# Performance work log

Hardware: AMD Instinct MI355X
Metric: run time of the kernel (lower is better)

## Reference

```python
import jax, jax.numpy as jnp
import numpy as np

BN_EPS = 1e-5


def _poly_ste(x):
    # Piecewise polynomial surrogate used for the activation STE backward:
    #   x < -1        -> -1
    #   x >= 1        -> 1
    out = jnp.where(x < -1, -1.0, x * x + 2.0 * x)
    out = jnp.where(x < 0, out, -x * x + 2.0 * x)
    out = jnp.where(x < 1, out, 1.0)
    return out


def setup_inputs() -> dict:
    key = jax.random.key(0)
    ks = jax.random.split(key, 7)
    N, C, H, W = 32, 128, 56, 56
    P = 128  # planes
    return {
        "x": jax.random.normal(ks[0], (N, C, H, W), dtype=jnp.float32),
        "weight": jax.random.normal(ks[1], (P, C, 3, 3), dtype=jnp.float32) * 0.05,
        "bias": jax.random.normal(ks[2], (P,), dtype=jnp.float32) * 0.05,
        "gamma": jax.random.uniform(ks[3], (P,), dtype=jnp.float32, minval=0.5, maxval=1.5),
        "beta": jax.random.normal(ks[4], (P,), dtype=jnp.float32) * 0.05,
        "running_mean": jax.random.normal(ks[5], (P,), dtype=jnp.float32) * 0.1,
        "running_var": jax.random.uniform(ks[6], (P,), dtype=jnp.float32, minval=0.5, maxval=1.5),
    }


def reference(x, weight, bias, gamma, beta, running_mean, running_var):
    # BinaryActivation: forward = sign(x), backward = d(poly)/dx (STE via detach trick)
    poly = _poly_ste(x)
    a = poly + jax.lax.stop_gradient(jnp.sign(x) - poly)

    # HardBinaryConv: weights binarized with straight-through sign; input already +/-1.
    wb = weight + jax.lax.stop_gradient(jnp.sign(weight) - weight)

    # 3x3 conv, stride 1, padding 1, NCHW / OIHW layout
    out = jax.lax.conv_general_dilated(
        a, wb,
        window_strides=(1, 1),
        padding=((1, 1), (1, 1)),
        dimension_numbers=("NCHW", "OIHW", "NCHW"),
    )
    out = out + bias[None, :, None, None]

    # BatchNorm2d in eval mode (running statistics)
    inv = gamma / jnp.sqrt(running_var + BN_EPS)
    out = out * inv[None, :, None, None] + (beta - running_mean * inv)[None, :, None, None]

    # Residual add (downsample=None, stride=1, inplanes==planes)
    return out + x
```

## Files before the change

kernel.cpp:

```cpp
#include <hip/hip_runtime.h>
#include <stdint.h>

#define N_  32
#define C_  128
#define H_  56
#define W_  56
#define HW_ 3136
#define P_  128

using i32x4 = __attribute__((ext_vector_type(4))) int;

#define WI8_BYTES (P_*1152)

__global__ __launch_bounds__(256) void wpack_kernel(const float* __restrict__ weight,
        const float* __restrict__ bias, const float* __restrict__ gamma,
        const float* __restrict__ beta, const float* __restrict__ mean,
        const float* __restrict__ var,
        uint32_t* __restrict__ wI8, float* __restrict__ invG, float* __restrict__ b0G) {
    int gid = blockIdx.x * 256 + threadIdx.x;
    int p   = gid / 288;
    int rem = gid % 288;
    int k   = rem * 4;
    int tp  = k >> 7;
    int c   = k & 127;
    uint32_t d = 0;
    #pragma unroll
    for (int i2 = 0; i2 < 4; ++i2) {
        float v = weight[((size_t)p * C_ + c + i2) * 9 + tp];
        uint32_t by = (v >= 0.f) ? 0x01u : 0xFFu;
        d |= by << (8 * i2);
    }
    wI8[gid] = d;
    if (blockIdx.x == 0 && threadIdx.x < P_) {
        int pp = threadIdx.x;
        float inv = gamma[pp] * rsqrtf(var[pp] + 1e-5f);
        invG[pp] = inv;
        b0G[pp]  = bias[pp] * inv + beta[pp] - mean[pp] * inv;
    }
}

__global__ __launch_bounds__(256) void bconv_kernel(
        const uint4* __restrict__ wI8v,
        const float* __restrict__ invG, const float* __restrict__ b0G,
        const float* __restrict__ x, float* __restrict__ out) {
    __shared__ uint4 actT[4 * 68 * 8];
    __shared__ float sInv[P_], sB0[P_];

    int tid = threadIdx.x;
    int bid = (blockIdx.x & 7) * 112 + (blockIdx.x >> 3);
    int img = bid / 28;
    int rp  = bid % 28;
    int r0  = rp * 2;

    int lane = tid & 63;
    int wi   = tid >> 6;
    int q    = lane >> 4;
    int l15  = lane & 15;
    int m0   = wi * 32;

    if (tid < P_) { sInv[tid] = invG[tid]; sB0[tid] = b0G[tid]; }

    const uint4* wbase = wI8v + (size_t)(m0 + l15) * 72;
    i32x4 aw[2][2][2];
    #pragma unroll
    for (int mi = 0; mi < 2; ++mi)
        #pragma unroll
        for (int ks = 0; ks < 2; ++ks)
            aw[0][mi][ks] = *(const i32x4*)&wI8v[(size_t)(m0 + mi*16 + l15) * 72
                                                 + ks * 4 + q];

    if (tid < 224) {
        int rho = tid / 56;
        int rr2 = tid % 56;
        int cg  = rr2 / 14;
        int tq  = rr2 % 14;
        int h   = r0 - 1 + rho;
        bool vh = ((unsigned)h < (unsigned)H_);
        uint32_t c0 = vh ? 0x01010101u : 0u;
        uint32_t cf = vh ? 0xFEu       : 0u;
        const uint32_t* xb = (const uint32_t*)x
            + ((size_t)img * C_ + cg * 32) * HW_ + (vh ? h : 0) * W_ + tq * 4;
        int colL0 = tq * 4 + 1;
        #pragma unroll
        for (int ph = 0; ph < 2; ++ph) {
            uint32_t cell0[4], cell1[4], cell2[4], cell3[4];
            #pragma unroll
            for (int d = 0; d < 4; ++d) {
                uint32_t w0 = 0, w1 = 0, w2 = 0, w3 = 0;
                if (vh) {
                    #pragma unroll
                    for (int i = 0; i < 4; ++i) {
                        uint4 u = *(const uint4*)(xb + (size_t)(ph * 16 + d * 4 + i) * HW_);
                        uint32_t sh = i * 8;
                        w0 |= (u.x >> 31) << sh;
                        w1 |= (u.y >> 31) << sh;
                        w2 |= (u.z >> 31) << sh;
                        w3 |= (u.w >> 31) << sh;
                    }
                }
                cell0[d] = c0 + w0 * cf;
                cell1[d] = c0 + w1 * cf;
                cell2[d] = c0 + w2 * cf;
                cell3[d] = c0 + w3 * cf;
            }
            int cb = cg * 2 + ph;
            actT[(rho * 68 + colL0 + 0) * 8 + (cb ^ ((colL0 + 0) & 7))] =
                make_uint4(cell0[0], cell0[1], cell0[2], cell0[3]);
            actT[(rho * 68 + colL0 + 1) * 8 + (cb ^ ((colL0 + 1) & 7))] =
                make_uint4(cell1[0], cell1[1], cell1[2], cell1[3]);
            actT[(rho * 68 + colL0 + 2) * 8 + (cb ^ ((colL0 + 2) & 7))] =
                make_uint4(cell2[0], cell2[1], cell2[2], cell2[3]);
            actT[(rho * 68 + colL0 + 3) * 8 + (cb ^ ((colL0 + 3) & 7))] =
                make_uint4(cell3[0], cell3[1], cell3[2], cell3[3]);
        }
    } else {
        int z = tid - 224;
        #pragma unroll
        for (int rep = 0; rep < 2; ++rep) {
            int e = z + rep * 32;
            if (e < 48) {
                int rho  = e / 12;
                int jj   = e % 12;
                int colL = jj ? (56 + jj) : 0;
                int base = (rho * 68 + colL) * 8;
                #pragma unroll
                for (int s = 0; s < 8; ++s) actT[base + s] = make_uint4(0u,0u,0u,0u);
            }
        }
    }

    __syncthreads();

    i32x4 acc[2][8];
    #pragma unroll
    for (int mi = 0; mi < 2; ++mi)
        #pragma unroll
        for (int j = 0; j < 8; ++j)
            #pragma unroll
            for (int e = 0; e < 4; ++e) acc[mi][j][e] = 0;

    #pragma unroll 1
    for (int t9 = 0; t9 < 9; ++t9) {
        int nb = t9 & 1;
        if (t9 < 8) {
            #pragma unroll
            for (int mi = 0; mi < 2; ++mi)
                #pragma unroll
                for (int ks = 0; ks < 2; ++ks)
                    aw[nb ^ 1][mi][ks] = *(const i32x4*)&wI8v[(size_t)(m0 + mi*16 + l15) * 72
                                                              + (t9 + 1) * 8 + ks * 4 + q];
        }
        int dh = t9 / 3, dw = t9 % 3;
        #pragma unroll
        for (int ks = 0; ks < 2; ++ks) {
            #pragma unroll
            for (int j = 0; j < 8; ++j) {
                int n    = j * 16 + l15;
                int colL = (n & 63) + dw;
                int rho  = (n >> 6) + dh;
                i32x4 bf = *(const i32x4*)&actT[(rho * 68 + colL) * 8 + ((ks * 4 + q) ^ (colL & 7))];
                acc[0][j] = __builtin_amdgcn_mfma_i32_16x16x64_i8(aw[nb][0][ks], bf, acc[0][j], 0, 0, 0);
                acc[1][j] = __builtin_amdgcn_mfma_i32_16x16x64_i8(aw[nb][1][ks], bf, acc[1][j], 0, 0, 0);
            }
        }
    }

    __syncthreads();

    float* S = (float*)actT + wi * (16 * 132);
    #pragma unroll
    for (int mi = 0; mi < 2; ++mi) {
        float invR[4], b0R[4];
        #pragma unroll
        for (int reg = 0; reg < 4; ++reg) {
            int m = m0 + mi * 16 + q * 4 + reg;
            invR[reg] = sInv[m];
            b0R[reg]  = sB0[m];
        }
        #pragma unroll
        for (int j = 0; j < 8; ++j) {
            int n = j * 16 + l15;
            #pragma unroll
            for (int reg = 0; reg < 4; ++reg)
                S[(q * 4 + reg) * 132 + n] = (float)acc[mi][j][reg] * invR[reg] + b0R[reg];
        }
        asm volatile("s_waitcnt lgkmcnt(0)" ::: "memory");
        if (lane < 56) {
            int ch4 = lane / 14;
            int wq  = lane % 14;
            #pragma unroll
            for (int k = 0; k < 4; ++k) {
                int chl = k * 4 + ch4;
                int ch  = m0 + mi * 16 + chl;
                #pragma unroll
                for (int rr2 = 0; rr2 < 2; ++rr2) {
                    float4 v = *(float4*)&S[chl * 132 + rr2 * 64 + wq * 4];
                    size_t off = (size_t)img * P_ * HW_ + (size_t)ch * HW_
                               + (size_t)(r0 + rr2) * W_ + wq * 4;
                    const float4 xr = *(const float4*)&x[off];
                    v.x += xr.x; v.y += xr.y; v.z += xr.z; v.w += xr.w;
                    *(float4*)&out[off] = v;
                }
            }
        }
        if (mi == 0)
            asm volatile("s_waitcnt lgkmcnt(0)" ::: "memory");
    }
}

extern "C" void kernel_launch(void* const* d_in, const int* in_sizes, int n_in,
                              void* d_out, int out_size, void* d_ws, size_t ws_size,
                              hipStream_t stream) {
    const float* x      = (const float*)d_in[0];
    const float* weight = (const float*)d_in[1];
    const float* bias   = (const float*)d_in[2];
    const float* gamma  = (const float*)d_in[3];
    const float* beta   = (const float*)d_in[4];
    const float* mean   = (const float*)d_in[5];
    const float* var    = (const float*)d_in[6];
    float* out = (float*)d_out;

    uint8_t*  ws    = (uint8_t*)d_ws;
    uint32_t* wI8   = (uint32_t*)ws;
    float*    invG  = (float*)(ws + WI8_BYTES);
    float*    b0G   = invG + P_;

    wpack_kernel<<<144, 256, 0, stream>>>(weight, bias, gamma, beta, mean, var, wI8, invG, b0G);
    bconv_kernel<<<32 * 28, 256, 0, stream>>>((const uint4*)wI8, invG, b0G, x, out);
}
```

Before: 149.8 us.

## Prepack binarized activations to workspace and DMA them into LDS

Adds a separate pack_act kernel that binarizes x into int8 rows, laid out already padded and swizzled in global workspace. The conv kernel then fills LDS with global_load_lds direct copies instead of binarizing per block. This removes the redundant re-reading of halo rows, since each block otherwise packs 4 rows for 2 output rows. The epilogue drops the LDS-staged float4 stores in favour of direct scalar stores, and unroll 1 is removed from the tap loop. The cost is an extra kernel launch, extra global traffic for the packed activations, and less coalesced output writes; a fallback path is kept for when the workspace is too small.

```diff
diff --git a/kernel.cpp b/kernel.cpp
--- a/kernel.cpp
+++ b/kernel.cpp
@@ -10,7 +10,10 @@
 
 using i32x4 = __attribute__((ext_vector_type(4))) int;
 
-#define WI8_BYTES (P_*1152)
+#define ACT_ROWB   8704
+#define ACT_NROWS  58
+#define ACT_BYTES  ((size_t)N_ * ACT_NROWS * ACT_ROWB)
+#define WI8_BYTES  (P_*1152)
 
 __global__ __launch_bounds__(256) void wpack_kernel(const float* __restrict__ weight,
         const float* __restrict__ bias, const float* __restrict__ gamma,
@@ -39,7 +42,152 @@
     }
 }
 
-__global__ __launch_bounds__(256) void bconv_kernel(
+__global__ __launch_bounds__(256) void pack_act(const float* __restrict__ x,
+                                                uint8_t* __restrict__ act) {
+    __shared__ uint32_t S[56 * 33];
+    int bid = blockIdx.x;
+    int n   = bid / ACT_NROWS, ridx = bid % ACT_NROWS;
+    int tid = threadIdx.x;
+    uint8_t* rowG = act + (size_t)bid * ACT_ROWB;
+    if (ridx == 0 || ridx == ACT_NROWS - 1) {
+        #pragma unroll
+        for (int j = 0; j < 3; ++j) {
+            int k = j * 256 + tid;
+            if (k < 544) *(uint4*)(rowG + (size_t)k * 16) = make_uint4(0u,0u,0u,0u);
+        }
+        return;
+    }
+    int h = ridx - 1;
+    const uint32_t* xb = (const uint32_t*)x + (size_t)n * C_ * HW_ + h * W_;
+    #pragma unroll
+    for (int j = 0; j < 7; ++j) {
+        int u  = j * 256 + tid;
+        int c4 = u / 56;
+        int w  = u - c4 * 56;
+        const uint32_t* p = xb + (size_t)(c4 * 4) * HW_ + w;
+        uint32_t s = (p[0] >> 31) | ((p[HW_] >> 31) << 8)
+                   | ((p[2 * HW_] >> 31) << 16) | ((p[3 * HW_] >> 31) << 24);
+        S[w * 33 + c4] = 0x01010101u + s * 0xFEu;
+    }
+    __syncthreads();
+    #pragma unroll
+    for (int j = 0; j < 3; ++j) {
+        int k = j * 256 + tid;
+        if (k < 544) {
+            int colL = k >> 3, cb = k & 7;
+            uint4 v = make_uint4(0u, 0u, 0u, 0u);
+            if (colL >= 1 && colL <= 56) {
+                int w = colL - 1;
+                v.x = S[w * 33 + cb * 4 + 0];
+                v.y = S[w * 33 + cb * 4 + 1];
+                v.z = S[w * 33 + cb * 4 + 2];
+                v.w = S[w * 33 + cb * 4 + 3];
+            }
+            int slot = cb ^ (colL & 7);
+            *(uint4*)(rowG + (size_t)(colL * 8 + slot) * 16) = v;
+        }
+    }
+}
+
+__global__ __launch_bounds__(256) void bconv_dma(
+        const uint4* __restrict__ wI8v,
+        const float* __restrict__ invG, const float* __restrict__ b0G,
+        const uint8_t* __restrict__ act,
+        const float* __restrict__ x, float* __restrict__ out) {
+    __shared__ uint4 actT[4 * 68 * 8];
+    __shared__ float sInv[P_], sB0[P_];
+
+    int tid = threadIdx.x;
+    int bid = (blockIdx.x & 7) * 112 + (blockIdx.x >> 3);
+    int img = bid / 28;
+    int rp  = bid % 28;
+    int r0  = rp * 2;
+
+    int lane = tid & 63;
+    int wi   = tid >> 6;
+    int q    = lane >> 4;
+    int l15  = lane & 15;
+    int m0   = wi * 32;
+
+    if (tid < P_) { sInv[tid] = invG[tid]; sB0[tid] = b0G[tid]; }
+
+    i32x4 aw[2][2][2];
+    #pragma unroll
+    for (int mi = 0; mi < 2; ++mi)
+        #pragma unroll
+        for (int ks = 0; ks < 2; ++ks)
+            aw[0][mi][ks] = *(const i32x4*)&wI8v[(size_t)(m0 + mi*16 + l15) * 72
+                                                 + ks * 4 + q];
+
+    const uint8_t* actG = act + (size_t)img * ACT_NROWS * ACT_ROWB;
+    #pragma unroll
+    for (int i = 0; i < 9; ++i) {
+        int cid = i * 256 + tid;
+        if (cid < 2176) {
+            int rho    = cid / 544;
+            int within = cid - rho * 544;
+            __builtin_amdgcn_global_load_lds(
+                (const uint32_t*)(actG + (size_t)(r0 + rho) * ACT_ROWB
+                                       + (size_t)within * 16),
+                (uint32_t*)&actT[cid], 16, 0, 0);
+        }
+    }
+
+    __syncthreads();
+
+    i32x4 acc[2][8];
+    #pragma unroll
+    for (int mi = 0; mi < 2; ++mi)
+        #pragma unroll
+        for (int j = 0; j < 8; ++j)
+            #pragma unroll
+            for (int e = 0; e < 4; ++e) acc[mi][j][e] = 0;
+
+    for (int t9 = 0; t9 < 9; ++t9) {
+        int nb = t9 & 1;
+        if (t9 < 8) {
+            #pragma unroll
+            for (int mi = 0; mi < 2; ++mi)
+                #pragma unroll
+                for (int ks = 0; ks < 2; ++ks)
+                    aw[nb ^ 1][mi][ks] = *(const i32x4*)&wI8v[(size_t)(m0 + mi*16 + l15) * 72
+                                                              + (t9 + 1) * 8 + ks * 4 + q];
+        }
+        int dh = t9 / 3, dw = t9 % 3;
+        #pragma unroll
+        for (int ks = 0; ks < 2; ++ks) {
+            #pragma unroll
+            for (int j = 0; j < 8; ++j) {
+                int n    = j * 16 + l15;
+                int colL = (n & 63) + dw;
+                int rho  = (n >> 6) + dh;
+                i32x4 bf = *(const i32x4*)&actT[(rho * 68 + colL) * 8 + ((ks * 4 + q) ^ (colL & 7))];
+                acc[0][j] = __builtin_amdgcn_mfma_i32_16x16x64_i8(aw[nb][0][ks], bf, acc[0][j], 0, 0, 0);
+                acc[1][j] = __builtin_amdgcn_mfma_i32_16x16x64_i8(aw[nb][1][ks], bf, acc[1][j], 0, 0, 0);
+            }
+        }
+    }
+
+    #pragma unroll
+    for (int j = 0; j < 8; ++j) {
+        int n = j * 16 + l15;
+        int w = n & 63;
+        if (w < W_) {
+            int orow = r0 + (n >> 6);
+            size_t pixOff = (size_t)img * P_ * HW_ + (size_t)orow * W_ + w;
+            #pragma unroll
+            for (int mi = 0; mi < 2; ++mi)
+                #pragma unroll
+                for (int reg = 0; reg < 4; ++reg) {
+                    int m = m0 + mi * 16 + q * 4 + reg;
+                    size_t off = pixOff + (size_t)m * HW_;
+                    out[off] = (float)acc[mi][j][reg] * sInv[m] + sB0[m] + x[off];
+                }
+        }
+    }
+}
+
+__global__ __launch_bounds__(256) void bconv_fused(
         const uint4* __restrict__ wI8v,
         const float* __restrict__ invG, const float* __restrict__ b0G,
         const float* __restrict__ x, float* __restrict__ out) {
@@ -60,7 +208,6 @@
 
     if (tid < P_) { sInv[tid] = invG[tid]; sB0[tid] = b0G[tid]; }
 
-    const uint4* wbase = wI8v + (size_t)(m0 + l15) * 72;
     i32x4 aw[2][2][2];
     #pragma unroll
     for (int mi = 0; mi < 2; ++mi)
@@ -139,7 +286,6 @@
             #pragma unroll
             for (int e = 0; e < 4; ++e) acc[mi][j][e] = 0;
 
-    #pragma unroll 1
     for (int t9 = 0; t9 < 9; ++t9) {
         int nb = t9 & 1;
         if (t9 < 8) {
@@ -165,46 +311,22 @@
         }
     }
 
-    __syncthreads();
-
-    float* S = (float*)actT + wi * (16 * 132);
-    #pragma unroll
-    for (int mi = 0; mi < 2; ++mi) {
-        float invR[4], b0R[4];
-        #pragma unroll
-        for (int reg = 0; reg < 4; ++reg) {
-            int m = m0 + mi * 16 + q * 4 + reg;
-            invR[reg] = sInv[m];
-            b0R[reg]  = sB0[m];
-        }
-        #pragma unroll
-        for (int j = 0; j < 8; ++j) {
-            int n = j * 16 + l15;
-            #pragma unroll
-            for (int reg = 0; reg < 4; ++reg)
-                S[(q * 4 + reg) * 132 + n] = (float)acc[mi][j][reg] * invR[reg] + b0R[reg];
-        }
-        asm volatile("s_waitcnt lgkmcnt(0)" ::: "memory");
-        if (lane < 56) {
-            int ch4 = lane / 14;
-            int wq  = lane % 14;
-            #pragma unroll
-            for (int k = 0; k < 4; ++k) {
-                int chl = k * 4 + ch4;
-                int ch  = m0 + mi * 16 + chl;
-                #pragma unroll
-                for (int rr2 = 0; rr2 < 2; ++rr2) {
-                    float4 v = *(float4*)&S[chl * 132 + rr2 * 64 + wq * 4];
-                    size_t off = (size_t)img * P_ * HW_ + (size_t)ch * HW_
-                               + (size_t)(r0 + rr2) * W_ + wq * 4;
-                    const float4 xr = *(const float4*)&x[off];
-                    v.x += xr.x; v.y += xr.y; v.z += xr.z; v.w += xr.w;
-                    *(float4*)&out[off] = v;
+    #pragma unroll
+    for (int j = 0; j < 8; ++j) {
+        int n = j * 16 + l15;
+        int w = n & 63;
+        if (w < W_) {
+            int orow = r0 + (n >> 6);
+            size_t pixOff = (size_t)img * P_ * HW_ + (size_t)orow * W_ + w;
+            #pragma unroll
+            for (int mi = 0; mi < 2; ++mi)
+                #pragma unroll
+                for (int reg = 0; reg < 4; ++reg) {
+                    int m = m0 + mi * 16 + q * 4 + reg;
+                    size_t off = pixOff + (size_t)m * HW_;
+                    out[off] = (float)acc[mi][j][reg] * sInv[m] + sB0[m] + x[off];
                 }
-            }
-        }
-        if (mi == 0)
-            asm volatile("s_waitcnt lgkmcnt(0)" ::: "memory");
+        }
     }
 }
 
@@ -220,11 +342,22 @@
     const float* var    = (const float*)d_in[6];
     float* out = (float*)d_out;
 
-    uint8_t*  ws    = (uint8_t*)d_ws;
-    uint32_t* wI8   = (uint32_t*)ws;
-    float*    invG  = (float*)(ws + WI8_BYTES);
-    float*    b0G   = invG + P_;
-
-    wpack_kernel<<<144, 256, 0, stream>>>(weight, bias, gamma, beta, mean, var, wI8, invG, b0G);
-    bconv_kernel<<<32 * 28, 256, 0, stream>>>((const uint4*)wI8, invG, b0G, x, out);
-}
+    uint8_t* ws = (uint8_t*)d_ws;
+    size_t need = ACT_BYTES + WI8_BYTES + 1024;
+
+    if (ws_size >= need) {
+        uint8_t*  act  = ws;
+        uint32_t* wI8  = (uint32_t*)(ws + ACT_BYTES);
+        float*    invG = (float*)(ws + ACT_BYTES + WI8_BYTES);
+        float*    b0G  = invG + P_;
+        pack_act<<<N_ * ACT_NROWS, 256, 0, stream>>>(x, act);
+        wpack_kernel<<<144, 256, 0, stream>>>(weight, bias, gamma, beta, mean, var, wI8, invG, b0G);
+        bconv_dma<<<32 * 28, 256, 0, stream>>>((const uint4*)wI8, invG, b0G, act, x, out);
+    } else {
+        uint32_t* wI8  = (uint32_t*)ws;
+        float*    invG = (float*)(ws + WI8_BYTES);
+        float*    b0G  = invG + P_;
+        wpack_kernel<<<144, 256, 0, stream>>>(weight, bias, gamma, beta, mean, var, wI8, invG, b0G);
+        bconv_fused<<<32 * 28, 256, 0, stream>>>((const uint4*)wI8, invG, b0G, x, out);
+    }
+}
```

New measurement: 147.4 us. About the same (-1.6%).
